# Kernel optimization log

Hardware: AMD Instinct MI355X
Metric: run time of the kernel (lower is better)

Reference implementation:

```python
import jax, jax.numpy as jnp
import numpy as np

B = 2048      # batch
C = 200       # n_country
F = 32        # n_feat_country == n_input
H = 256       # n_hidden


def setup_inputs() -> dict:
    key = jax.random.key(0)
    ks = jax.random.split(key, 9)
    x = jax.random.normal(ks[0], (B, C * F), dtype=jnp.float32)
    transition = jax.random.uniform(ks[1], (C, C), dtype=jnp.float32) / C
    W1 = jax.random.normal(ks[2], (F, H), dtype=jnp.float32) * (1.0 / np.sqrt(F))
    b1 = jax.random.normal(ks[3], (H,), dtype=jnp.float32) * 0.01
    W2 = jax.random.normal(ks[4], (H, H), dtype=jnp.float32) * (1.0 / np.sqrt(H))
    b2 = jax.random.normal(ks[5], (H,), dtype=jnp.float32) * 0.01
    W3 = jax.random.normal(ks[6], (H, 1), dtype=jnp.float32) * (1.0 / np.sqrt(H))
    b3 = jax.random.normal(ks[7], (1,), dtype=jnp.float32) * 0.01
    return {"x": x, "transition": transition, "W1": W1, "b1": b1,
            "W2": W2, "b2": b2, "W3": W3, "b3": b3}


def reference(x, transition, W1, b1, W2, b2, W3, b3):
    Bsz, N = x.shape
    Cn = transition.shape[0]
    Ff = N // Cn
    xc = x.reshape(Bsz, Cn, Ff)            # per-country feature blocks
    S = xc[..., 0]                          # [B, C] susceptible (feature 0)
    I = xc[..., 1]                          # [B, C] infected   (feature 1)
    # transition-weighted neighbor aggregation (the python loop == one GEMM)
    sinflow = S @ transition                # [B, C]
    iinflow = I @ transition                # [B, C]
    outflow = 1.0 - jnp.diag(transition)    # [C]
    # shared tiny MLP applied per country (vectorized over C)
    h = jax.nn.relu(jnp.einsum('bcf,fh->bch', xc, W1) + b1)
    h = jax.nn.relu(jnp.einsum('bch,hk->bck', h, W2) + b2)
    lamb = (jnp.einsum('bch,ho->bco', h, W3) + b3)[..., 0]  # [B, C]
    dS = -lamb * S + sinflow - outflow * S
    dI = lamb * S + iinflow - outflow * I
    # interleave: pred[:, 2i] = S_i + dS_i, pred[:, 2i+1] = I_i + dI_i
    pred = jnp.stack([S + dS, I + dI], axis=-1).reshape(Bsz, 2 * Cn)
    return pred
```

## Files before the change

### kernel.cpp

```cpp
#include <hip/hip_runtime.h>
#include <stdint.h>

#define M_ROWS 409600
#define B_CNT  2048
#define C_CNT  200
#define N_TILES (M_ROWS / 64)
#define GRID_MLP 512

typedef __attribute__((ext_vector_type(8))) short bf16x8;
typedef __attribute__((ext_vector_type(4))) float f32x4;

__device__ __forceinline__ ushort f2bf(float f) {
    uint32_t u = __float_as_uint(f);
    u += 0x7fffu + ((u >> 16) & 1u);
    return (ushort)(u >> 16);
}

__device__ __forceinline__ uint32_t cvtpk_bf16(float lo, float hi) {
    uint32_t r;
    asm("v_cvt_pk_bf16_f32 %0, %1, %2" : "=v"(r) : "v"(lo), "v"(hi));
    return r;
}

__device__ __forceinline__ f32x4 mfma16(bf16x8 a, bf16x8 b, f32x4 c) {
    return __builtin_amdgcn_mfma_f32_16x16x32_bf16(a, b, c, 0, 0, 0);
}

__device__ __forceinline__ bf16x8 pack8(float4 a, float4 b) {
    bf16x8 r;
    r[0] = (short)f2bf(a.x); r[1] = (short)f2bf(a.y);
    r[2] = (short)f2bf(a.z); r[3] = (short)f2bf(a.w);
    r[4] = (short)f2bf(b.x); r[5] = (short)f2bf(b.y);
    r[6] = (short)f2bf(b.z); r[7] = (short)f2bf(b.w);
    return r;
}

__global__ __launch_bounds__(256) void prep_kernel(
    const float* __restrict__ x, const float* __restrict__ T,
    const float* __restrict__ W1, const float* __restrict__ W2,
    ushort* __restrict__ xb16, float4* __restrict__ epi,
    ushort* __restrict__ W1t, ushort* __restrict__ W2t, int do_xb) {
    int blk = blockIdx.x, t = threadIdx.x;
    if (blk < B_CNT) {
        __shared__ float Sr[C_CNT], Ir[C_CNT];
        const float4* xr = (const float4*)(x + (size_t)blk * 6400);
        ushort4* xw = (ushort4*)(xb16 + (size_t)blk * 6400);
#pragma unroll
        for (int i = 0; i < 7; ++i) {
            int i4 = i * 256 + t;
            if (i4 < 1600) {
                float4 v = xr[i4];
                if (do_xb) {
                    ushort4 u;
                    u.x = f2bf(v.x); u.y = f2bf(v.y);
                    u.z = f2bf(v.z); u.w = f2bf(v.w);
                    xw[i4] = u;
                }
                if ((i4 & 7) == 0) {
                    int c = i4 >> 3;
                    Sr[c] = v.x; Ir[c] = v.y;
                }
            }
        }
        __syncthreads();
        if (t < C_CNT) {
            float as = 0.f, ai = 0.f;
            for (int cp = 0; cp < C_CNT; ++cp) {
                float tv = T[cp * C_CNT + t];
                as = fmaf(Sr[cp], tv, as);
                ai = fmaf(Ir[cp], tv, ai);
            }
            float S = Sr[t], I = Ir[t];
            float of = 1.0f - T[t * C_CNT + t];
            float4 e;
            e.x = S;
            e.y = S + as - of * S;
            e.z = I + ai - of * I;
            e.w = 0.f;
            epi[(size_t)blk * C_CNT + t] = e;
        }
    } else if (blk < B_CNT + 256) {
        int n = blk - B_CNT;
        W2t[n * 256 + t] = f2bf(W2[t * 256 + n]);
    } else {
        int idx = (blk - B_CNT - 256) * 256 + t;
        int n = idx >> 5, k = idx & 31;
        W1t[idx] = f2bf(W1[k * 256 + n]);
    }
}

template <bool XB>
__global__ __launch_bounds__(256, 2) void mlp_kernel(
    const float* __restrict__ x,
    const ushort* __restrict__ xb16,
    const float* __restrict__ b1,
    const float* __restrict__ b2,
    const float* __restrict__ W3,
    const float* __restrict__ b3,
    const ushort* __restrict__ W1t,
    const ushort* __restrict__ W2t,
    const float4* __restrict__ epi,
    float* __restrict__ out) {
    constexpr int RS = 264;
    __shared__ ushort h1s[2][64 * RS];
    __shared__ float b1f[256], b2f[256], w3f[256];
    __shared__ float lamb2[2][4][64];

    const int tid  = threadIdx.x;
    const int w    = tid >> 6;
    const int lane = tid & 63;
    const int L    = lane & 15;
    const int q    = lane >> 4;

    b1f[tid] = b1[tid];
    b2f[tid] = b2[tid];
    w3f[tid] = W3[tid];
    const float b3v = b3[0];

    bf16x8 a2r[4][8];
#pragma unroll
    for (int i2 = 0; i2 < 4; ++i2)
#pragma unroll
        for (int kc = 0; kc < 8; ++kc)
            a2r[i2][kc] =
                *(const bf16x8*)(W2t + (64 * w + i2 * 16 + L) * 256 + kc * 32 + q * 8);

    uint32_t w1off = (uint32_t)(((64 * w + L) * 32 + q * 8) * sizeof(ushort));

    int tile = blockIdx.x;
    bf16x8 bx[4];
#pragma unroll
    for (int i = 0; i < 4; ++i) {
        if (XB) {
            bx[i] = *(const bf16x8*)(xb16 + (size_t)(tile * 64 + i * 16 + L) * 32 + q * 8);
        } else {
            const float4* xr =
                (const float4*)(x + (size_t)(tile * 64 + i * 16 + L) * 32 + q * 8);
            bx[i] = pack8(xr[0], xr[1]);
        }
    }

    float eS = 0.f, eP = 0.f, eQ = 0.f;
    int ptile = -1;
    int buf = 0, wp = 0;

    __syncthreads();

    for (; tile < N_TILES; tile += GRID_MLP) {
        asm volatile("" : "+v"(w1off));
        const char* w1p = (const char*)W1t + w1off;
#pragma unroll
        for (int c = 0; c < 2; ++c) {
            bf16x8 aw[2];
#pragma unroll
            for (int i = 0; i < 2; ++i)
                aw[i] = *(const bf16x8*)(w1p + (size_t)(c * 2 + i) * 1024);

            f32x4 acc1[2][4];
#pragma unroll
            for (int i1 = 0; i1 < 2; ++i1)
#pragma unroll
                for (int im = 0; im < 4; ++im)
                    acc1[i1][im] = mfma16(aw[i1], bx[im], (f32x4){0.f, 0.f, 0.f, 0.f});

#pragma unroll
            for (int i1 = 0; i1 < 2; ++i1) {
                int n1b = 64 * w + (c * 2 + i1) * 16 + q * 4;
                const float4 bv = *reinterpret_cast<const float4*>(&b1f[n1b]);
#pragma unroll
                for (int im = 0; im < 4; ++im) {
                    int m = im * 16 + L;
                    float v0 = fmaxf(acc1[i1][im][0] + bv.x, 0.f);
                    float v1 = fmaxf(acc1[i1][im][1] + bv.y, 0.f);
                    float v2 = fmaxf(acc1[i1][im][2] + bv.z, 0.f);
                    float v3 = fmaxf(acc1[i1][im][3] + bv.w, 0.f);
                    uint2 pk;
                    pk.x = cvtpk_bf16(v0, v1);
                    pk.y = cvtpk_bf16(v2, v3);
                    *reinterpret_cast<uint2*>(&h1s[buf][m * RS + n1b]) = pk;
                }
            }
        }

        __syncthreads();

        if (ptile >= 0 && tid < 64) {
            int gm = ptile * 64 + tid;
            float lam = lamb2[wp ^ 1][0][tid] + lamb2[wp ^ 1][1][tid] +
                        lamb2[wp ^ 1][2][tid] + lamb2[wp ^ 1][3][tid] + b3v;
            float2 o;
            o.x = eP - lam * eS;
            o.y = eQ + lam * eS;
            ((float2*)out)[gm] = o;
        }

        f32x4 acc2[4][4];
#pragma unroll
        for (int i2 = 0; i2 < 4; ++i2)
#pragma unroll
            for (int im = 0; im < 4; ++im) acc2[i2][im] = (f32x4){0.f, 0.f, 0.f, 0.f};

#pragma unroll
        for (int kc = 0; kc < 8; ++kc) {
            bf16x8 bh[4];
#pragma unroll
            for (int im = 0; im < 4; ++im) {
                int m = im * 16 + L;
                bh[im] = *(const bf16x8*)(&h1s[buf][m * RS + kc * 32 + q * 8]);
            }
#pragma unroll
            for (int i2 = 0; i2 < 4; ++i2)
#pragma unroll
                for (int im = 0; im < 4; ++im)
                    acc2[i2][im] = mfma16(a2r[i2][kc], bh[im], acc2[i2][im]);
        }

        {
            int tn = tile + GRID_MLP;
            if (tn >= N_TILES) tn = tile;
            const size_t mn0 = (size_t)tn * 64;
#pragma unroll
            for (int i = 0; i < 4; ++i) {
                if (XB) {
                    bx[i] = *(const bf16x8*)(xb16 + (mn0 + i * 16 + L) * 32 + q * 8);
                } else {
                    const float4* xr =
                        (const float4*)(x + (mn0 + i * 16 + L) * 32 + q * 8);
                    bx[i] = pack8(xr[0], xr[1]);
                }
            }
        }

        if (tid < 64) {
            float4 e = epi[(size_t)tile * 64 + tid];
            eS = e.x; eP = e.y; eQ = e.z;
        }

        float part[4] = {0.f, 0.f, 0.f, 0.f};
#pragma unroll
        for (int i2 = 0; i2 < 4; ++i2) {
            int n2b = 64 * w + i2 * 16 + q * 4;
            const float4 b2v = *reinterpret_cast<const float4*>(&b2f[n2b]);
            const float4 w3v = *reinterpret_cast<const float4*>(&w3f[n2b]);
#pragma unroll
            for (int im = 0; im < 4; ++im) {
                float h0 = fmaxf(acc2[i2][im][0] + b2v.x, 0.f);
                float h1 = fmaxf(acc2[i2][im][1] + b2v.y, 0.f);
                float h2 = fmaxf(acc2[i2][im][2] + b2v.z, 0.f);
                float h3 = fmaxf(acc2[i2][im][3] + b2v.w, 0.f);
                part[im] = fmaf(h0, w3v.x, part[im]);
                part[im] = fmaf(h1, w3v.y, part[im]);
                part[im] = fmaf(h2, w3v.z, part[im]);
                part[im] = fmaf(h3, w3v.w, part[im]);
            }
        }

#pragma unroll
        for (int im = 0; im < 4; ++im) {
            float pp = part[im];
            pp += __shfl_xor(pp, 16);
            pp += __shfl_xor(pp, 32);
            if (q == 0) lamb2[wp][w][im * 16 + L] = pp;
        }

        ptile = tile;
        buf ^= 1;
        wp ^= 1;
    }

    __syncthreads();
    if (ptile >= 0 && tid < 64) {
        int gm = ptile * 64 + tid;
        float lam = lamb2[wp ^ 1][0][tid] + lamb2[wp ^ 1][1][tid] +
                    lamb2[wp ^ 1][2][tid] + lamb2[wp ^ 1][3][tid] + b3v;
        float2 o;
        o.x = eP - lam * eS;
        o.y = eQ + lam * eS;
        ((float2*)out)[gm] = o;
    }
}

extern "C" void kernel_launch(void* const* d_in, const int* in_sizes, int n_in,
                              void* d_out, int out_size, void* d_ws, size_t ws_size,
                              hipStream_t stream) {
    const float* x  = (const float*)d_in[0];
    const float* T  = (const float*)d_in[1];
    const float* W1 = (const float*)d_in[2];
    const float* b1 = (const float*)d_in[3];
    const float* W2 = (const float*)d_in[4];
    const float* b2 = (const float*)d_in[5];
    const float* W3 = (const float*)d_in[6];
    const float* b3 = (const float*)d_in[7];

    const size_t xb_bytes = (size_t)M_ROWS * 32 * 2;
    const size_t epi_b    = (size_t)M_ROWS * 16;
    const size_t small    = epi_b + 8192 * 2 + 65536 * 2;
    const int    do_xb    = (ws_size >= xb_bytes + small) ? 1 : 0;

    char* ws = (char*)d_ws;
    ushort* xb16 = (ushort*)ws;
    char* base = ws + (do_xb ? xb_bytes : 0);
    float4* epi  = (float4*)(base);
    ushort* W1t  = (ushort*)(base + epi_b);
    ushort* W2t  = (ushort*)(base + epi_b + 8192 * 2);

    hipLaunchKernelGGL(prep_kernel, dim3(B_CNT + 256 + 32), dim3(256), 0, stream,
                       x, T, W1, W2, xb16, epi, W1t, W2t, do_xb);
    if (do_xb) {
        hipLaunchKernelGGL((mlp_kernel<true>), dim3(GRID_MLP), dim3(256), 0, stream,
                           x, xb16, b1, b2, W3, b3, W1t, W2t, epi, (float*)d_out);
    } else {
        hipLaunchKernelGGL((mlp_kernel<false>), dim3(GRID_MLP), dim3(256), 0, stream,
                           x, xb16, b1, b2, W3, b3, W1t, W2t, epi, (float*)d_out);
    }
}
```

Measured before the change: 174.3 us.

## Process two row tiles per MLP loop iteration to halve block barriers

Restructures the persistent MLP loop so each block handles two 64-row tiles per iteration, with the layer-1 fronts of both tiles written to separate shared buffers before a single barrier. The layer-2/3 GEMMs then run back-to-back, with the next x-tile loads and epilogue loads interleaved between them, and the lambda staging array is widened to hold two tiles. The intent is to cut the per-tile __syncthreads and pipeline bubbles and to expose more independent MFMA work. In exchange, an extra set of input registers and epilogue values is held live on top of the register-resident W2 fragments, which risks spills under the 2-blocks-per-CU launch bound. A tail path is added for the odd leftover tile.

```diff
diff --git a/kernel.cpp b/kernel.cpp
--- a/kernel.cpp
+++ b/kernel.cpp
@@ -9,6 +9,8 @@
 
 typedef __attribute__((ext_vector_type(8))) short bf16x8;
 typedef __attribute__((ext_vector_type(4))) float f32x4;
+
+constexpr int RS = 264;
 
 __device__ __forceinline__ ushort f2bf(float f) {
     uint32_t u = __float_as_uint(f);
@@ -90,6 +92,117 @@
 }
 
 template <bool XB>
+__device__ __forceinline__ void load_bx(bf16x8 (&bx)[4],
+                                        const ushort* __restrict__ xb16,
+                                        const float* __restrict__ x,
+                                        int t, int L, int q) {
+#pragma unroll
+    for (int i = 0; i < 4; ++i) {
+        if (XB) {
+            bx[i] = *(const bf16x8*)(xb16 + (size_t)(t * 64 + i * 16 + L) * 32 + q * 8);
+        } else {
+            const float4* xr =
+                (const float4*)(x + (size_t)(t * 64 + i * 16 + L) * 32 + q * 8);
+            bx[i] = pack8(xr[0], xr[1]);
+        }
+    }
+}
+
+__device__ __forceinline__ void tile_front(
+    uint32_t& w1off, const ushort* __restrict__ W1t, const bf16x8 (&bx)[4],
+    ushort* __restrict__ h1buf, const float* __restrict__ b1f,
+    int w, int L, int q) {
+    asm volatile("" : "+v"(w1off));
+    const char* w1p = (const char*)W1t + w1off;
+#pragma unroll
+    for (int c = 0; c < 2; ++c) {
+        bf16x8 aw[2];
+#pragma unroll
+        for (int i = 0; i < 2; ++i)
+            aw[i] = *(const bf16x8*)(w1p + (size_t)(c * 2 + i) * 1024);
+
+        f32x4 acc1[2][4];
+#pragma unroll
+        for (int i1 = 0; i1 < 2; ++i1)
+#pragma unroll
+            for (int im = 0; im < 4; ++im)
+                acc1[i1][im] = mfma16(aw[i1], bx[im], (f32x4){0.f, 0.f, 0.f, 0.f});
+
+#pragma unroll
+        for (int i1 = 0; i1 < 2; ++i1) {
+            int n1b = 64 * w + (c * 2 + i1) * 16 + q * 4;
+            const float4 bv = *reinterpret_cast<const float4*>(&b1f[n1b]);
+#pragma unroll
+            for (int im = 0; im < 4; ++im) {
+                int m = im * 16 + L;
+                float v0 = fmaxf(acc1[i1][im][0] + bv.x, 0.f);
+                float v1 = fmaxf(acc1[i1][im][1] + bv.y, 0.f);
+                float v2 = fmaxf(acc1[i1][im][2] + bv.z, 0.f);
+                float v3 = fmaxf(acc1[i1][im][3] + bv.w, 0.f);
+                uint2 pk;
+                pk.x = cvtpk_bf16(v0, v1);
+                pk.y = cvtpk_bf16(v2, v3);
+                *reinterpret_cast<uint2*>(&h1buf[m * RS + n1b]) = pk;
+            }
+        }
+    }
+}
+
+__device__ __forceinline__ void tile_gemm2(
+    const bf16x8 (&a2r)[4][8], const ushort* __restrict__ h1buf,
+    f32x4 (&acc2)[4][4], int L, int q) {
+#pragma unroll
+    for (int i2 = 0; i2 < 4; ++i2)
+#pragma unroll
+        for (int im = 0; im < 4; ++im) acc2[i2][im] = (f32x4){0.f, 0.f, 0.f, 0.f};
+#pragma unroll
+    for (int kc = 0; kc < 8; ++kc) {
+        bf16x8 bh[4];
+#pragma unroll
+        for (int im = 0; im < 4; ++im) {
+            int m = im * 16 + L;
+            bh[im] = *(const bf16x8*)(&h1buf[m * RS + kc * 32 + q * 8]);
+        }
+#pragma unroll
+        for (int i2 = 0; i2 < 4; ++i2)
+#pragma unroll
+            for (int im = 0; im < 4; ++im)
+                acc2[i2][im] = mfma16(a2r[i2][kc], bh[im], acc2[i2][im]);
+    }
+}
+
+__device__ __forceinline__ void tile_gemm3(
+    const f32x4 (&acc2)[4][4], const float* __restrict__ b2f,
+    const float* __restrict__ w3f, float (*__restrict__ ls)[64],
+    int w, int L, int q) {
+    float part[4] = {0.f, 0.f, 0.f, 0.f};
+#pragma unroll
+    for (int i2 = 0; i2 < 4; ++i2) {
+        int n2b = 64 * w + i2 * 16 + q * 4;
+        const float4 b2v = *reinterpret_cast<const float4*>(&b2f[n2b]);
+        const float4 w3v = *reinterpret_cast<const float4*>(&w3f[n2b]);
+#pragma unroll
+        for (int im = 0; im < 4; ++im) {
+            float h0 = fmaxf(acc2[i2][im][0] + b2v.x, 0.f);
+            float h1 = fmaxf(acc2[i2][im][1] + b2v.y, 0.f);
+            float h2 = fmaxf(acc2[i2][im][2] + b2v.z, 0.f);
+            float h3 = fmaxf(acc2[i2][im][3] + b2v.w, 0.f);
+            part[im] = fmaf(h0, w3v.x, part[im]);
+            part[im] = fmaf(h1, w3v.y, part[im]);
+            part[im] = fmaf(h2, w3v.z, part[im]);
+            part[im] = fmaf(h3, w3v.w, part[im]);
+        }
+    }
+#pragma unroll
+    for (int im = 0; im < 4; ++im) {
+        float pp = part[im];
+        pp += __shfl_xor(pp, 16);
+        pp += __shfl_xor(pp, 32);
+        if (q == 0) ls[w][im * 16 + L] = pp;
+    }
+}
+
+template <bool XB>
 __global__ __launch_bounds__(256, 2) void mlp_kernel(
     const float* __restrict__ x,
     const ushort* __restrict__ xb16,
@@ -101,10 +214,9 @@
     const ushort* __restrict__ W2t,
     const float4* __restrict__ epi,
     float* __restrict__ out) {
-    constexpr int RS = 264;
     __shared__ ushort h1s[2][64 * RS];
     __shared__ float b1f[256], b2f[256], w3f[256];
-    __shared__ float lamb2[2][4][64];
+    __shared__ float lamb2[2][2][4][64];
 
     const int tid  = threadIdx.x;
     const int w    = tid >> 6;
@@ -128,155 +240,117 @@
     uint32_t w1off = (uint32_t)(((64 * w + L) * 32 + q * 8) * sizeof(ushort));
 
     int tile = blockIdx.x;
-    bf16x8 bx[4];
-#pragma unroll
-    for (int i = 0; i < 4; ++i) {
-        if (XB) {
-            bx[i] = *(const bf16x8*)(xb16 + (size_t)(tile * 64 + i * 16 + L) * 32 + q * 8);
-        } else {
-            const float4* xr =
-                (const float4*)(x + (size_t)(tile * 64 + i * 16 + L) * 32 + q * 8);
-            bx[i] = pack8(xr[0], xr[1]);
-        }
-    }
-
-    float eS = 0.f, eP = 0.f, eQ = 0.f;
-    int ptile = -1;
-    int buf = 0, wp = 0;
+    bf16x8 bxa[4], bxb[4];
+    load_bx<XB>(bxa, xb16, x, tile, L, q);
+    load_bx<XB>(bxb, xb16, x, tile + GRID_MLP, L, q);
+
+    float eSa = 0.f, ePa = 0.f, eQa = 0.f;
+    float eSb = 0.f, ePb = 0.f, eQb = 0.f;
+    int pta = -1, ptb = -1;
+    int wp = 0;
 
     __syncthreads();
 
-    for (; tile < N_TILES; tile += GRID_MLP) {
-        asm volatile("" : "+v"(w1off));
-        const char* w1p = (const char*)W1t + w1off;
-#pragma unroll
-        for (int c = 0; c < 2; ++c) {
-            bf16x8 aw[2];
-#pragma unroll
-            for (int i = 0; i < 2; ++i)
-                aw[i] = *(const bf16x8*)(w1p + (size_t)(c * 2 + i) * 1024);
-
-            f32x4 acc1[2][4];
-#pragma unroll
-            for (int i1 = 0; i1 < 2; ++i1)
-#pragma unroll
-                for (int im = 0; im < 4; ++im)
-                    acc1[i1][im] = mfma16(aw[i1], bx[im], (f32x4){0.f, 0.f, 0.f, 0.f});
-
-#pragma unroll
-            for (int i1 = 0; i1 < 2; ++i1) {
-                int n1b = 64 * w + (c * 2 + i1) * 16 + q * 4;
-                const float4 bv = *reinterpret_cast<const float4*>(&b1f[n1b]);
-#pragma unroll
-                for (int im = 0; im < 4; ++im) {
-                    int m = im * 16 + L;
-                    float v0 = fmaxf(acc1[i1][im][0] + bv.x, 0.f);
-                    float v1 = fmaxf(acc1[i1][im][1] + bv.y, 0.f);
-                    float v2 = fmaxf(acc1[i1][im][2] + bv.z, 0.f);
-                    float v3 = fmaxf(acc1[i1][im][3] + bv.w, 0.f);
-                    uint2 pk;
-                    pk.x = cvtpk_bf16(v0, v1);
-                    pk.y = cvtpk_bf16(v2, v3);
-                    *reinterpret_cast<uint2*>(&h1s[buf][m * RS + n1b]) = pk;
-                }
-            }
-        }
+    for (; tile + GRID_MLP < N_TILES; tile += 2 * GRID_MLP) {
+        const int ta = tile, tb = tile + GRID_MLP;
+
+        tile_front(w1off, W1t, bxa, &h1s[0][0], b1f, w, L, q);
+        tile_front(w1off, W1t, bxb, &h1s[1][0], b1f, w, L, q);
 
         __syncthreads();
 
-        if (ptile >= 0 && tid < 64) {
-            int gm = ptile * 64 + tid;
-            float lam = lamb2[wp ^ 1][0][tid] + lamb2[wp ^ 1][1][tid] +
-                        lamb2[wp ^ 1][2][tid] + lamb2[wp ^ 1][3][tid] + b3v;
-            float2 o;
-            o.x = eP - lam * eS;
-            o.y = eQ + lam * eS;
-            ((float2*)out)[gm] = o;
-        }
-
-        f32x4 acc2[4][4];
-#pragma unroll
-        for (int i2 = 0; i2 < 4; ++i2)
-#pragma unroll
-            for (int im = 0; im < 4; ++im) acc2[i2][im] = (f32x4){0.f, 0.f, 0.f, 0.f};
-
-#pragma unroll
-        for (int kc = 0; kc < 8; ++kc) {
-            bf16x8 bh[4];
-#pragma unroll
-            for (int im = 0; im < 4; ++im) {
-                int m = im * 16 + L;
-                bh[im] = *(const bf16x8*)(&h1s[buf][m * RS + kc * 32 + q * 8]);
-            }
-#pragma unroll
-            for (int i2 = 0; i2 < 4; ++i2)
-#pragma unroll
-                for (int im = 0; im < 4; ++im)
-                    acc2[i2][im] = mfma16(a2r[i2][kc], bh[im], acc2[i2][im]);
-        }
-
-        {
-            int tn = tile + GRID_MLP;
-            if (tn >= N_TILES) tn = tile;
-            const size_t mn0 = (size_t)tn * 64;
-#pragma unroll
-            for (int i = 0; i < 4; ++i) {
-                if (XB) {
-                    bx[i] = *(const bf16x8*)(xb16 + (mn0 + i * 16 + L) * 32 + q * 8);
-                } else {
-                    const float4* xr =
-                        (const float4*)(x + (mn0 + i * 16 + L) * 32 + q * 8);
-                    bx[i] = pack8(xr[0], xr[1]);
-                }
-            }
-        }
-
-        if (tid < 64) {
-            float4 e = epi[(size_t)tile * 64 + tid];
-            eS = e.x; eP = e.y; eQ = e.z;
-        }
-
-        float part[4] = {0.f, 0.f, 0.f, 0.f};
-#pragma unroll
-        for (int i2 = 0; i2 < 4; ++i2) {
-            int n2b = 64 * w + i2 * 16 + q * 4;
-            const float4 b2v = *reinterpret_cast<const float4*>(&b2f[n2b]);
-            const float4 w3v = *reinterpret_cast<const float4*>(&w3f[n2b]);
-#pragma unroll
-            for (int im = 0; im < 4; ++im) {
-                float h0 = fmaxf(acc2[i2][im][0] + b2v.x, 0.f);
-                float h1 = fmaxf(acc2[i2][im][1] + b2v.y, 0.f);
-                float h2 = fmaxf(acc2[i2][im][2] + b2v.z, 0.f);
-                float h3 = fmaxf(acc2[i2][im][3] + b2v.w, 0.f);
-                part[im] = fmaf(h0, w3v.x, part[im]);
-                part[im] = fmaf(h1, w3v.y, part[im]);
-                part[im] = fmaf(h2, w3v.z, part[im]);
-                part[im] = fmaf(h3, w3v.w, part[im]);
-            }
-        }
-
-#pragma unroll
-        for (int im = 0; im < 4; ++im) {
-            float pp = part[im];
-            pp += __shfl_xor(pp, 16);
-            pp += __shfl_xor(pp, 32);
-            if (q == 0) lamb2[wp][w][im * 16 + L] = pp;
-        }
-
-        ptile = tile;
-        buf ^= 1;
-        wp ^= 1;
+        if (pta >= 0 && tid < 64) {
+            {
+                float lam = lamb2[wp ^ 1][0][0][tid] + lamb2[wp ^ 1][0][1][tid] +
+                            lamb2[wp ^ 1][0][2][tid] + lamb2[wp ^ 1][0][3][tid] + b3v;
+                float2 o; o.x = ePa - lam * eSa; o.y = eQa + lam * eSa;
+                ((float2*)out)[pta * 64 + tid] = o;
+            }
+            {
+                float lam = lamb2[wp ^ 1][1][0][tid] + lamb2[wp ^ 1][1][1][tid] +
+                            lamb2[wp ^ 1][1][2][tid] + lamb2[wp ^ 1][1][3][tid] + b3v;
+                float2 o; o.x = ePb - lam * eSb; o.y = eQb + lam * eSb;
+                ((float2*)out)[ptb * 64 + tid] = o;
+            }
+        }
+
+        {
+            f32x4 acc2[4][4];
+            tile_gemm2(a2r, &h1s[0][0], acc2, L, q);
+            tile_gemm3(acc2, b2f, w3f, lamb2[wp][0], w, L, q);
+        }
+        {
+            int tna = tile + 2 * GRID_MLP;
+            if (tna >= N_TILES) tna = ta;
+            load_bx<XB>(bxa, xb16, x, tna, L, q);
+        }
+        __builtin_amdgcn_sched_barrier(0);
+
+        {
+            f32x4 acc2[4][4];
+            tile_gemm2(a2r, &h1s[1][0], acc2, L, q);
+            if (tid < 64) {
+                float4 ea = epi[(size_t)ta * 64 + tid];
+                float4 eb = epi[(size_t)tb * 64 + tid];
+                eSa = ea.x; ePa = ea.y; eQa = ea.z;
+                eSb = eb.x; ePb = eb.y; eQb = eb.z;
+            }
+            tile_gemm3(acc2, b2f, w3f, lamb2[wp][1], w, L, q);
+        }
+        {
+            int tnb = tile + 3 * GRID_MLP;
+            if (tnb >= N_TILES) tnb = ta;
+            load_bx<XB>(bxb, xb16, x, tnb, L, q);
+        }
+
+        pta = ta; ptb = tb; wp ^= 1;
+
+        __syncthreads();
+    }
+
+    if (tile < N_TILES) {
+        tile_front(w1off, W1t, bxa, &h1s[0][0], b1f, w, L, q);
+        __syncthreads();
+        if (pta >= 0 && tid < 64) {
+            {
+                float lam = lamb2[wp ^ 1][0][0][tid] + lamb2[wp ^ 1][0][1][tid] +
+                            lamb2[wp ^ 1][0][2][tid] + lamb2[wp ^ 1][0][3][tid] + b3v;
+                float2 o; o.x = ePa - lam * eSa; o.y = eQa + lam * eSa;
+                ((float2*)out)[pta * 64 + tid] = o;
+            }
+            {
+                float lam = lamb2[wp ^ 1][1][0][tid] + lamb2[wp ^ 1][1][1][tid] +
+                            lamb2[wp ^ 1][1][2][tid] + lamb2[wp ^ 1][1][3][tid] + b3v;
+                float2 o; o.x = ePb - lam * eSb; o.y = eQb + lam * eSb;
+                ((float2*)out)[ptb * 64 + tid] = o;
+            }
+        }
+        {
+            f32x4 acc2[4][4];
+            tile_gemm2(a2r, &h1s[0][0], acc2, L, q);
+            if (tid < 64) {
+                float4 ea = epi[(size_t)tile * 64 + tid];
+                eSa = ea.x; ePa = ea.y; eQa = ea.z;
+            }
+            tile_gemm3(acc2, b2f, w3f, lamb2[wp][0], w, L, q);
+        }
+        pta = tile; ptb = -1; wp ^= 1;
     }
 
     __syncthreads();
-    if (ptile >= 0 && tid < 64) {
-        int gm = ptile * 64 + tid;
-        float lam = lamb2[wp ^ 1][0][tid] + lamb2[wp ^ 1][1][tid] +
-                    lamb2[wp ^ 1][2][tid] + lamb2[wp ^ 1][3][tid] + b3v;
-        float2 o;
-        o.x = eP - lam * eS;
-        o.y = eQ + lam * eS;
-        ((float2*)out)[gm] = o;
+    if (pta >= 0 && tid < 64) {
+        {
+            float lam = lamb2[wp ^ 1][0][0][tid] + lamb2[wp ^ 1][0][1][tid] +
+                        lamb2[wp ^ 1][0][2][tid] + lamb2[wp ^ 1][0][3][tid] + b3v;
+            float2 o; o.x = ePa - lam * eSa; o.y = eQa + lam * eSa;
+            ((float2*)out)[pta * 64 + tid] = o;
+        }
+        if (ptb >= 0) {
+            float lam = lamb2[wp ^ 1][1][0][tid] + lamb2[wp ^ 1][1][1][tid] +
+                        lamb2[wp ^ 1][1][2][tid] + lamb2[wp ^ 1][1][3][tid] + b3v;
+            float2 o; o.x = ePb - lam * eSb; o.y = eQb + lam * eSb;
+            ((float2*)out)[ptb * 64 + tid] = o;
+        }
     }
 }
 
```

After: 184.3 us. 1.06x slower.

## Drop bf16 x staging copy and batch transition GEMM over 8 rows per block

Applied to the files above, without the earlier changes.

Stops the prep kernel from writing a full bf16 copy of x. The MLP kernel now always reads fp32 x directly and converts it with packed v_cvt_pk_bf16 instructions. The prep kernel reads only the S/I pairs, and each block handles 8 batch rows so every transition load is reused 8 times. The aim is to remove a large extra write-and-read pass over x and cut redundant transition traffic, at the cost of the MLP kernel reading twice as many bytes for x.

```diff
diff --git a/kernel.cpp b/kernel.cpp
--- a/kernel.cpp
+++ b/kernel.cpp
@@ -6,9 +6,11 @@
 #define C_CNT  200
 #define N_TILES (M_ROWS / 64)
 #define GRID_MLP 512
+#define RPB     8
 
 typedef __attribute__((ext_vector_type(8))) short bf16x8;
 typedef __attribute__((ext_vector_type(4))) float f32x4;
+
 
 __device__ __forceinline__ ushort f2bf(float f) {
     uint32_t u = __float_as_uint(f);
@@ -26,73 +28,71 @@
     return __builtin_amdgcn_mfma_f32_16x16x32_bf16(a, b, c, 0, 0, 0);
 }
 
-__device__ __forceinline__ bf16x8 pack8(float4 a, float4 b) {
-    bf16x8 r;
-    r[0] = (short)f2bf(a.x); r[1] = (short)f2bf(a.y);
-    r[2] = (short)f2bf(a.z); r[3] = (short)f2bf(a.w);
-    r[4] = (short)f2bf(b.x); r[5] = (short)f2bf(b.y);
-    r[6] = (short)f2bf(b.z); r[7] = (short)f2bf(b.w);
-    return r;
+__device__ __forceinline__ bf16x8 pack8f(const float4* __restrict__ xr) {
+    float4 a = xr[0], b = xr[1];
+    union { bf16x8 v; uint32_t u[4]; } r;
+    r.u[0] = cvtpk_bf16(a.x, a.y);
+    r.u[1] = cvtpk_bf16(a.z, a.w);
+    r.u[2] = cvtpk_bf16(b.x, b.y);
+    r.u[3] = cvtpk_bf16(b.z, b.w);
+    return r.v;
 }
 
 __global__ __launch_bounds__(256) void prep_kernel(
     const float* __restrict__ x, const float* __restrict__ T,
     const float* __restrict__ W1, const float* __restrict__ W2,
-    ushort* __restrict__ xb16, float4* __restrict__ epi,
-    ushort* __restrict__ W1t, ushort* __restrict__ W2t, int do_xb) {
+    float4* __restrict__ epi,
+    ushort* __restrict__ W1t, ushort* __restrict__ W2t) {
     int blk = blockIdx.x, t = threadIdx.x;
-    if (blk < B_CNT) {
-        __shared__ float Sr[C_CNT], Ir[C_CNT];
-        const float4* xr = (const float4*)(x + (size_t)blk * 6400);
-        ushort4* xw = (ushort4*)(xb16 + (size_t)blk * 6400);
-#pragma unroll
-        for (int i = 0; i < 7; ++i) {
-            int i4 = i * 256 + t;
-            if (i4 < 1600) {
-                float4 v = xr[i4];
-                if (do_xb) {
-                    ushort4 u;
-                    u.x = f2bf(v.x); u.y = f2bf(v.y);
-                    u.z = f2bf(v.z); u.w = f2bf(v.w);
-                    xw[i4] = u;
-                }
-                if ((i4 & 7) == 0) {
-                    int c = i4 >> 3;
-                    Sr[c] = v.x; Ir[c] = v.y;
-                }
+    if (blk < 256) {
+        __shared__ float Sr[C_CNT][RPB];
+        __shared__ float Ir[C_CNT][RPB];
+        if (t < C_CNT) {
+#pragma unroll
+            for (int r = 0; r < RPB; ++r) {
+                const float2 si =
+                    *(const float2*)(x + (size_t)(blk * RPB + r) * 6400 + t * 32);
+                Sr[t][r] = si.x;
+                Ir[t][r] = si.y;
             }
         }
         __syncthreads();
         if (t < C_CNT) {
-            float as = 0.f, ai = 0.f;
+            float as[RPB], ai[RPB];
+#pragma unroll
+            for (int r = 0; r < RPB; ++r) { as[r] = 0.f; ai[r] = 0.f; }
             for (int cp = 0; cp < C_CNT; ++cp) {
                 float tv = T[cp * C_CNT + t];
-                as = fmaf(Sr[cp], tv, as);
-                ai = fmaf(Ir[cp], tv, ai);
-            }
-            float S = Sr[t], I = Ir[t];
+#pragma unroll
+                for (int r = 0; r < RPB; ++r) {
+                    as[r] = fmaf(Sr[cp][r], tv, as[r]);
+                    ai[r] = fmaf(Ir[cp][r], tv, ai[r]);
+                }
+            }
             float of = 1.0f - T[t * C_CNT + t];
-            float4 e;
-            e.x = S;
-            e.y = S + as - of * S;
-            e.z = I + ai - of * I;
-            e.w = 0.f;
-            epi[(size_t)blk * C_CNT + t] = e;
-        }
-    } else if (blk < B_CNT + 256) {
-        int n = blk - B_CNT;
+#pragma unroll
+            for (int r = 0; r < RPB; ++r) {
+                float S = Sr[t][r], I = Ir[t][r];
+                float4 e;
+                e.x = S;
+                e.y = S + as[r] - of * S;
+                e.z = I + ai[r] - of * I;
+                e.w = 0.f;
+                epi[(size_t)(blk * RPB + r) * C_CNT + t] = e;
+            }
+        }
+    } else if (blk < 512) {
+        int n = blk - 256;
         W2t[n * 256 + t] = f2bf(W2[t * 256 + n]);
     } else {
-        int idx = (blk - B_CNT - 256) * 256 + t;
+        int idx = (blk - 512) * 256 + t;
         int n = idx >> 5, k = idx & 31;
         W1t[idx] = f2bf(W1[k * 256 + n]);
     }
 }
 
-template <bool XB>
 __global__ __launch_bounds__(256, 2) void mlp_kernel(
     const float* __restrict__ x,
-    const ushort* __restrict__ xb16,
     const float* __restrict__ b1,
     const float* __restrict__ b2,
     const float* __restrict__ W3,
@@ -130,15 +130,8 @@
     int tile = blockIdx.x;
     bf16x8 bx[4];
 #pragma unroll
-    for (int i = 0; i < 4; ++i) {
-        if (XB) {
-            bx[i] = *(const bf16x8*)(xb16 + (size_t)(tile * 64 + i * 16 + L) * 32 + q * 8);
-        } else {
-            const float4* xr =
-                (const float4*)(x + (size_t)(tile * 64 + i * 16 + L) * 32 + q * 8);
-            bx[i] = pack8(xr[0], xr[1]);
-        }
-    }
+    for (int i = 0; i < 4; ++i)
+        bx[i] = pack8f((const float4*)(x + (size_t)(tile * 64 + i * 16 + L) * 32 + q * 8));
 
     float eS = 0.f, eP = 0.f, eQ = 0.f;
     int ptile = -1;
@@ -220,15 +213,8 @@
             if (tn >= N_TILES) tn = tile;
             const size_t mn0 = (size_t)tn * 64;
 #pragma unroll
-            for (int i = 0; i < 4; ++i) {
-                if (XB) {
-                    bx[i] = *(const bf16x8*)(xb16 + (mn0 + i * 16 + L) * 32 + q * 8);
-                } else {
-                    const float4* xr =
-                        (const float4*)(x + (mn0 + i * 16 + L) * 32 + q * 8);
-                    bx[i] = pack8(xr[0], xr[1]);
-                }
-            }
+            for (int i = 0; i < 4; ++i)
+                bx[i] = pack8f((const float4*)(x + (mn0 + i * 16 + L) * 32 + q * 8));
         }
 
         if (tid < 64) {
@@ -292,25 +278,14 @@
     const float* W3 = (const float*)d_in[6];
     const float* b3 = (const float*)d_in[7];
 
-    const size_t xb_bytes = (size_t)M_ROWS * 32 * 2;
-    const size_t epi_b    = (size_t)M_ROWS * 16;
-    const size_t small    = epi_b + 8192 * 2 + 65536 * 2;
-    const int    do_xb    = (ws_size >= xb_bytes + small) ? 1 : 0;
-
+    const size_t epi_b = (size_t)M_ROWS * 16;
     char* ws = (char*)d_ws;
-    ushort* xb16 = (ushort*)ws;
-    char* base = ws + (do_xb ? xb_bytes : 0);
-    float4* epi  = (float4*)(base);
-    ushort* W1t  = (ushort*)(base + epi_b);
-    ushort* W2t  = (ushort*)(base + epi_b + 8192 * 2);
-
-    hipLaunchKernelGGL(prep_kernel, dim3(B_CNT + 256 + 32), dim3(256), 0, stream,
-                       x, T, W1, W2, xb16, epi, W1t, W2t, do_xb);
-    if (do_xb) {
-        hipLaunchKernelGGL((mlp_kernel<true>), dim3(GRID_MLP), dim3(256), 0, stream,
-                           x, xb16, b1, b2, W3, b3, W1t, W2t, epi, (float*)d_out);
-    } else {
-        hipLaunchKernelGGL((mlp_kernel<false>), dim3(GRID_MLP), dim3(256), 0, stream,
-                           x, xb16, b1, b2, W3, b3, W1t, W2t, epi, (float*)d_out);
-    }
-}
+    float4* epi  = (float4*)(ws);
+    ushort* W1t  = (ushort*)(ws + epi_b);
+    ushort* W2t  = (ushort*)(ws + epi_b + 8192 * 2);
+
+    hipLaunchKernelGGL(prep_kernel, dim3(256 + 256 + 32), dim3(256), 0, stream,
+                       x, T, W1, W2, epi, W1t, W2t);
+    hipLaunchKernelGGL(mlp_kernel, dim3(GRID_MLP), dim3(256), 0, stream,
+                       x, b1, b2, W3, b3, W1t, W2t, epi, (float*)d_out);
+}
```

New measurement: 178.3 us. 2.3% more time.
